# Kernel tuning notes

Hardware: AMD Instinct MI355X
Metric: run time of the kernel (lower is better)

The kernel has to match this reference:

```python
import jax, jax.numpy as jnp
import numpy as np

NUM_HEADS = 4
HEAD_DIM = 64
BN_EPS = 1e-5


def setup_inputs() -> dict:
    key = jax.random.key(0)
    ks = jax.random.split(key, 6)
    B, C, H, W = 8, 256, 48, 48
    HD = NUM_HEADS * HEAD_DIM  # 256
    x = jax.random.normal(ks[0], (B, C, H, W), dtype=jnp.float32)
    q_w = jax.random.normal(ks[1], (HD, C), dtype=jnp.float32) * (1.0 / np.sqrt(C))
    k_w = jax.random.normal(ks[2], (HEAD_DIM, C), dtype=jnp.float32) * (1.0 / np.sqrt(C))
    v_w = jax.random.normal(ks[3], (HEAD_DIM, C), dtype=jnp.float32) * (1.0 / np.sqrt(C))
    proj_w = jax.random.normal(ks[4], (C, HD), dtype=jnp.float32) * (1.0 / np.sqrt(HD))
    proj_b = jnp.zeros((C,), dtype=jnp.float32)
    gamma = jnp.ones((C,), dtype=jnp.float32)
    beta = jnp.zeros((C,), dtype=jnp.float32)
    return {"x": x, "q_w": q_w, "k_w": k_w, "v_w": v_w,
            "proj_w": proj_w, "proj_b": proj_b, "gamma": gamma, "beta": beta}


def reference(x, q_w, k_w, v_w, proj_w, proj_b, gamma, beta):
    B, C, H, W = x.shape
    N = H * W
    scale = HEAD_DIM ** -0.5
    xf = x.reshape(B, C, N)  # 1x1 conv == channel matmul
    q = jnp.einsum('oc,bcn->bon', q_w, xf).reshape(B, NUM_HEADS, HEAD_DIM, N)
    k = jnp.einsum('dc,bcn->bdn', k_w, xf)  # shared single KV head (MQA)
    v = jnp.einsum('dc,bcn->bdn', v_w, xf)
    # scores: [B, heads, N, N]
    attn = jnp.einsum('bhdn,bdm->bhnm', q, k) * scale
    attn = jax.nn.softmax(attn, axis=-1)
    out = jnp.einsum('bhnm,bdm->bhdn', attn, v)  # [B, heads, d, N]
    out = out.reshape(B, NUM_HEADS * HEAD_DIM, N)
    out = jnp.einsum('co,bon->bcn', proj_w, out) + proj_b[None, :, None]
    out = out.reshape(B, C, H, W)
    # BatchNorm2d (training-mode batch statistics, biased variance)
    mean = jnp.mean(out, axis=(0, 2, 3), keepdims=True)
    var = jnp.var(out, axis=(0, 2, 3), keepdims=True)
    out = gamma[None, :, None, None] * (out - mean) * jax.lax.rsqrt(var + BN_EPS) + beta[None, :, None, None]
    return out + x
```

## Files before the change

kernel.cpp:

```cpp
#include <hip/hip_runtime.h>
#include <hip/hip_bf16.h>
#include <math.h>

#define BB 8
#define CCH 256
#define NN 2304
#define NH 4
#define HDIM 64
#define QKV_ROWS 384
#define BN_EPS 1e-5f
#define NTILES 36
#define NPART 288
#define SLOG2E 0.18033688011112042f

typedef short bf16x8 __attribute__((ext_vector_type(8)));
typedef short bf16x4 __attribute__((ext_vector_type(4)));
typedef float f32x4 __attribute__((ext_vector_type(4)));

#if __has_builtin(__builtin_amdgcn_exp2f)
#define EXP2(x) __builtin_amdgcn_exp2f(x)
#else
#define EXP2(x) __expf((x) * 0.6931471805599453f)
#endif

#define MFMA32(a, b, c) __builtin_amdgcn_mfma_f32_16x16x32_bf16(a, b, c, 0, 0, 0)

__device__ __forceinline__ unsigned bfpair(float a, float b) {
    __hip_bfloat162 h = __float22bfloat162_rn(make_float2(a, b));
    return *(unsigned*)&h;
}
__device__ __forceinline__ unsigned short f2bf(float f) {
    unsigned u = __float_as_uint(f);
    u = (u + 0x7FFFu + ((u >> 16) & 1u)) >> 16;
    return (unsigned short)u;
}
__device__ __forceinline__ float bf2f(unsigned short s) {
    return __uint_as_float((unsigned)s << 16);
}

__global__ __launch_bounds__(256) void prep_k(
    const float* __restrict__ x,
    const float* __restrict__ qw, const float* __restrict__ kw,
    const float* __restrict__ vw, const float* __restrict__ pw,
    unsigned short* __restrict__ xT, unsigned short* __restrict__ xb,
    unsigned short* __restrict__ Wb, unsigned short* __restrict__ Pb)
{
    const int bid = blockIdx.x;
    const int tid = threadIdx.x;
    if (bid < 1152) {
        __shared__ float sX[64][65];
        const int b  = bid / 144;
        const int rem = bid - b * 144;
        const int nb = (rem >> 2) * 64;
        const int cb = (rem & 3) * 64;

        #pragma unroll
        for (int u = 0; u < 4; ++u) {
            int c  = (tid >> 4) + 16 * u;
            int n4 = (tid & 15) * 4;
            float4 v = *(const float4*)(x + ((size_t)(b * CCH + cb + c)) * NN + nb + n4);
            sX[c][n4+0] = v.x; sX[c][n4+1] = v.y; sX[c][n4+2] = v.z; sX[c][n4+3] = v.w;
        }
        __syncthreads();

        const int n  = tid >> 2;
        const int cg = (tid & 3) * 16;
        unsigned vals[8];
        #pragma unroll
        for (int p = 0; p < 8; ++p)
            vals[p] = bfpair(sX[cg + 2*p][n], sX[cg + 2*p + 1][n]);
        unsigned short* dst = xT + ((size_t)(b * NN + nb + n)) * CCH + cb + cg;
        *(uint4*)dst = make_uint4(vals[0], vals[1], vals[2], vals[3]);
        *(uint4*)(dst + 8) = make_uint4(vals[4], vals[5], vals[6], vals[7]);

        #pragma unroll
        for (int it = 0; it < 2; ++it) {
            int flat = tid + 256 * it;
            int row = flat >> 3;
            int n8  = (flat & 7) * 8;
            unsigned vv[4];
            #pragma unroll
            for (int p = 0; p < 4; ++p)
                vv[p] = bfpair(sX[row][n8 + 2*p], sX[row][n8 + 2*p + 1]);
            *(uint4*)(xb + ((size_t)(b * CCH + cb + row)) * NN + nb + n8) =
                make_uint4(vv[0], vv[1], vv[2], vv[3]);
        }
    } else {
        int idx = (bid - 1152) * 256 + tid;
        if (idx < 98304) {
            int o = idx >> 8, c = idx & 255;
            float v;
            if (o < 256)      v = qw[(size_t)o * CCH + c] * SLOG2E;
            else if (o < 320) v = kw[(size_t)(o - 256) * CCH + c];
            else              v = vw[(size_t)(o - 320) * CCH + c];
            Wb[idx] = f2bf(v);
        } else {
            int j = idx - 98304;
            if (j < 65536) Pb[j] = f2bf(pw[j]);
        }
    }
}

__global__ __launch_bounds__(128) void qkv_mfma_k(
    const unsigned short* __restrict__ Wb, const unsigned short* __restrict__ xT,
    unsigned short* __restrict__ Qt, unsigned short* __restrict__ Kt,
    unsigned short* __restrict__ Vn)
{
    __shared__ unsigned short sE[2][64 * 72];
    const int tid = threadIdx.x;
    const int wave = tid >> 6;
    const int lane = tid & 63;
    const int quad = lane >> 4;
    const int l15  = lane & 15;
    const int b  = blockIdx.x;
    const int nb = blockIdx.y * 64;
    const int mb = blockIdx.z * 128 + wave * 64;

    const unsigned short* Ab = Wb + (size_t)(mb + l15) * CCH + quad * 8;
    const unsigned short* Bb = xT + ((size_t)(b * NN + nb + l15)) * CCH + quad * 8;

    f32x4 C[4][4] = {};
    bf16x8 aA[2][4], bB[2][4];
    #pragma unroll
    for (int i = 0; i < 4; ++i) aA[0][i] = *(const bf16x8*)(Ab + (size_t)(16*i) * CCH);
    #pragma unroll
    for (int j = 0; j < 4; ++j) bB[0][j] = *(const bf16x8*)(Bb + (size_t)(16*j) * CCH);

    #pragma unroll
    for (int kk = 0; kk < 8; ++kk) {
        const int cur = kk & 1;
        if (kk < 7) {
            const int k1 = (kk + 1) * 32;
            #pragma unroll
            for (int i = 0; i < 4; ++i) aA[cur^1][i] = *(const bf16x8*)(Ab + (size_t)(16*i) * CCH + k1);
            #pragma unroll
            for (int j = 0; j < 4; ++j) bB[cur^1][j] = *(const bf16x8*)(Bb + (size_t)(16*j) * CCH + k1);
        }
        #pragma unroll
        for (int i = 0; i < 4; ++i)
            #pragma unroll
            for (int j = 0; j < 4; ++j)
                C[i][j] = MFMA32(aA[cur][i], bB[cur][j], C[i][j]);
    }

    unsigned short* sEw = &sE[wave][0];
    if (mb < 320) {
        #pragma unroll
        for (int i = 0; i < 4; ++i)
            #pragma unroll
            for (int j = 0; j < 4; ++j) {
                unsigned p01 = bfpair(C[i][j][0], C[i][j][1]);
                unsigned p23 = bfpair(C[i][j][2], C[i][j][3]);
                unsigned short* p = sEw + (16*j + l15) * 72 + 16*i + quad*4;
                *(unsigned*)p = p01;
                *(unsigned*)(p + 2) = p23;
            }
        if (mb < 256) {
            #pragma unroll
            for (int it = 0; it < 8; ++it) {
                int flat = lane + 64 * it;
                int row = flat >> 3;
                int o8  = (flat & 7) * 8;
                uint4 v = *(const uint4*)(sEw + row * 72 + o8);
                *(uint4*)(Qt + ((size_t)(b * NN + nb + row)) * CCH + mb + o8) = v;
            }
        } else {
            #pragma unroll
            for (int it = 0; it < 8; ++it) {
                int flat = lane + 64 * it;
                int row = flat >> 3;
                int o8  = (flat & 7) * 8;
                uint4 v = *(const uint4*)(sEw + row * 72 + o8);
                *(uint4*)(Kt + ((size_t)(b * NN + nb + row)) * 64 + o8) = v;
            }
        }
    } else {
        #pragma unroll
        for (int i = 0; i < 4; ++i)
            #pragma unroll
            for (int j = 0; j < 4; ++j) {
                unsigned p01 = bfpair(C[i][j][0], C[i][j][1]);
                unsigned p23 = bfpair(C[i][j][2], C[i][j][3]);
                unsigned short* p = sEw + (16*i + quad*4) * 72 + 16*j + l15;
                p[0]   = (unsigned short)p01;
                p[72]  = (unsigned short)(p01 >> 16);
                p[144] = (unsigned short)p23;
                p[216] = (unsigned short)(p23 >> 16);
            }
        #pragma unroll
        for (int it = 0; it < 8; ++it) {
            int flat = lane + 64 * it;
            int row = flat >> 3;
            int n8  = (flat & 7) * 8;
            uint4 v = *(const uint4*)(sEw + row * 72 + n8);
            *(uint4*)(Vn + ((size_t)(b * 64 + (mb - 320) + row)) * NN + nb + n8) = v;
        }
    }
}

__global__ __launch_bounds__(256, 4) void attn_k(
    const unsigned short* __restrict__ Qt,
    const unsigned short* __restrict__ Kt,
    const unsigned short* __restrict__ Vn,
    unsigned short* __restrict__ Ao)
{
    __shared__ __align__(16) unsigned short sKV[2 * 2 * 64 * 64];

    const int tid   = threadIdx.x;
    const int wave  = tid >> 6;
    const int lane  = tid & 63;
    const int quad  = lane >> 4;
    const int l15   = lane & 15;
    const int qoff  = wave * 32;
    const int b     = blockIdx.x;
    const int nb    = blockIdx.y * 128;
    const int head  = blockIdx.z;

    const bf16x8 vone8 = {(short)0x3F80, (short)0x3F80, (short)0x3F80, (short)0x3F80,
                          (short)0x3F80, (short)0x3F80, (short)0x3F80, (short)0x3F80};

    bf16x8 bQ[2][2];
    const unsigned short* QtB = Qt + ((size_t)(b * NN + nb + qoff + l15)) * CCH + head * 64 + quad * 8;
    #pragma unroll
    for (int qt = 0; qt < 2; ++qt)
        #pragma unroll
        for (int s = 0; s < 2; ++s)
            bQ[qt][s] = *(const bf16x8*)(QtB + (size_t)(16*qt) * CCH + s * 32);

    const int r0  = tid >> 3;
    const int c8  = (tid & 7) * 8;
    const int kr0 = (r0 & 3) | (((r0 >> 3) & 3) << 2) | (((r0 >> 2) & 1) << 4);
    const int kwc = ((tid & 7) ^ (kr0 & 7)) * 8;
    const int vwc = ((tid & 7) ^ (r0 & 7)) * 8;

    const unsigned short* Kb = Kt + ((size_t)(b * NN + r0)) * 64 + c8;
    const unsigned short* Vb = Vn + ((size_t)(b * 64 + r0)) * NN + c8;

    bf16x8 pf[4];
    pf[0] = *(const bf16x8*)(Kb);
    pf[1] = *(const bf16x8*)(Kb + (size_t)32 * 64);
    pf[2] = *(const bf16x8*)(Vb);
    pf[3] = *(const bf16x8*)(Vb + (size_t)32 * NN);
    *(bf16x8*)(sKV + kr0 * 64 + kwc)          = pf[0];
    *(bf16x8*)(sKV + (kr0 + 32) * 64 + kwc)   = pf[1];
    *(bf16x8*)(sKV + 4096 + r0 * 64 + vwc)    = pf[2];
    *(bf16x8*)(sKV + 4096 + (r0 + 32) * 64 + vwc) = pf[3];
    pf[0] = *(const bf16x8*)(Kb + (size_t)64 * 64);
    pf[1] = *(const bf16x8*)(Kb + (size_t)96 * 64);
    pf[2] = *(const bf16x8*)(Vb + 64);
    pf[3] = *(const bf16x8*)(Vb + (size_t)32 * NN + 64);

    f32x4 O[4][2] = {};
    f32x4 dacc[2] = {};

    for (int step = 0; step < NTILES; ++step) {
        const int cur = step & 1;
        __syncthreads();

        if (step + 1 < NTILES) {
            unsigned short* dstb = sKV + (cur ^ 1) * 8192;
            *(bf16x8*)(dstb + kr0 * 64 + kwc)             = pf[0];
            *(bf16x8*)(dstb + (kr0 + 32) * 64 + kwc)      = pf[1];
            *(bf16x8*)(dstb + 4096 + r0 * 64 + vwc)       = pf[2];
            *(bf16x8*)(dstb + 4096 + (r0 + 32) * 64 + vwc) = pf[3];
        }
        if (step + 2 < NTILES) {
            const int keys0 = (step + 2) * 64;
            pf[0] = *(const bf16x8*)(Kb + (size_t)keys0 * 64);
            pf[1] = *(const bf16x8*)(Kb + (size_t)(keys0 + 32) * 64);
            pf[2] = *(const bf16x8*)(Vb + keys0);
            pf[3] = *(const bf16x8*)(Vb + (size_t)32 * NN + keys0);
        }

        const unsigned short* sKb = sKV + cur * 8192;
        const unsigned short* sVb = sKb + 4096;

        f32x4 C[4][2] = {};
        #pragma unroll
        for (int s = 0; s < 2; ++s)
            #pragma unroll
            for (int kt = 0; kt < 4; ++kt) {
                const int row = 16*kt + l15;
                const int chsw = ((s*4 + quad) ^ (row & 7)) * 8;
                bf16x8 aK = *(const bf16x8*)(sKb + row * 64 + chsw);
                C[kt][0] = MFMA32(aK, bQ[0][s], C[kt][0]);
                C[kt][1] = MFMA32(aK, bQ[1][s], C[kt][1]);
            }

        bf16x8 bP[2][2];
        #pragma unroll
        for (int kt2 = 0; kt2 < 2; ++kt2)
            #pragma unroll
            for (int qt = 0; qt < 2; ++qt) {
                union { unsigned u[4]; bf16x8 v; } xp;
                const f32x4 c0 = C[2*kt2][qt];
                const f32x4 c1 = C[2*kt2+1][qt];
                xp.u[0] = bfpair(EXP2(c0[0]), EXP2(c0[1]));
                xp.u[1] = bfpair(EXP2(c0[2]), EXP2(c0[3]));
                xp.u[2] = bfpair(EXP2(c1[0]), EXP2(c1[1]));
                xp.u[3] = bfpair(EXP2(c1[2]), EXP2(c1[3]));
                bP[kt2][qt] = xp.v;
            }

        #pragma unroll
        for (int kt2 = 0; kt2 < 2; ++kt2) {
            dacc[0] = MFMA32(vone8, bP[kt2][0], dacc[0]);
            dacc[1] = MFMA32(vone8, bP[kt2][1], dacc[1]);
        }

        #pragma unroll
        for (int jd = 0; jd < 4; ++jd)
            #pragma unroll
            for (int kt2 = 0; kt2 < 2; ++kt2) {
                const int row = 16*jd + l15;
                const int chsw = ((4*kt2 + quad) ^ (row & 7)) * 8;
                bf16x8 aV = *(const bf16x8*)(sVb + row * 64 + chsw);
                O[jd][0] = MFMA32(aV, bP[kt2][0], O[jd][0]);
                O[jd][1] = MFMA32(aV, bP[kt2][1], O[jd][1]);
            }
    }
    __syncthreads();

    float rinv[2];
    rinv[0] = 1.0f / dacc[0][0];
    rinv[1] = 1.0f / dacc[1][0];
    unsigned short* sT = (unsigned short*)sKV;
    #pragma unroll
    for (int qt = 0; qt < 2; ++qt)
        #pragma unroll
        for (int jd = 0; jd < 4; ++jd) {
            unsigned lo = bfpair(O[jd][qt][0] * rinv[qt], O[jd][qt][1] * rinv[qt]);
            unsigned hi = bfpair(O[jd][qt][2] * rinv[qt], O[jd][qt][3] * rinv[qt]);
            *(uint2*)(sT + (qoff + 16*qt + l15) * 72 + 16*jd + quad*4) = make_uint2(lo, hi);
        }
    __syncthreads();

    #pragma unroll
    for (int it = 0; it < 4; ++it) {
        int flat = tid + 256 * it;
        int row  = flat >> 3;
        int cc8  = (flat & 7) * 8;
        uint4 v = *(const uint4*)(sT + row * 72 + cc8);
        *(uint4*)(Ao + ((size_t)(b * NN + nb + row)) * CCH + head * 64 + cc8) = v;
    }
}

__global__ __launch_bounds__(128) void proj_mfma_k(
    const unsigned short* __restrict__ Pb, const unsigned short* __restrict__ Ao,
    const float* __restrict__ pb, unsigned short* __restrict__ projb,
    float* __restrict__ psum, float* __restrict__ psq)
{
    __shared__ unsigned short sE[2][64 * 72];
    const int tid = threadIdx.x;
    const int wave = tid >> 6;
    const int lane = tid & 63;
    const int quad = lane >> 4;
    const int l15  = lane & 15;
    const int b  = blockIdx.x;
    const int nb = blockIdx.y * 64;
    const int mb = blockIdx.z * 128 + wave * 64;
    const int part = b * NTILES + blockIdx.y;

    const unsigned short* Ab = Pb + (size_t)(mb + l15) * CCH + quad * 8;
    const unsigned short* Bb = Ao + ((size_t)(b * NN + nb + l15)) * CCH + quad * 8;

    f32x4 C[4][4] = {};
    bf16x8 aA[2][4], bB[2][4];
    #pragma unroll
    for (int i = 0; i < 4; ++i) aA[0][i] = *(const bf16x8*)(Ab + (size_t)(16*i) * CCH);
    #pragma unroll
    for (int j = 0; j < 4; ++j) bB[0][j] = *(const bf16x8*)(Bb + (size_t)(16*j) * CCH);

    #pragma unroll
    for (int kk = 0; kk < 8; ++kk) {
        const int cur = kk & 1;
        if (kk < 7) {
            const int k1 = (kk + 1) * 32;
            #pragma unroll
            for (int i = 0; i < 4; ++i) aA[cur^1][i] = *(const bf16x8*)(Ab + (size_t)(16*i) * CCH + k1);
            #pragma unroll
            for (int j = 0; j < 4; ++j) bB[cur^1][j] = *(const bf16x8*)(Bb + (size_t)(16*j) * CCH + k1);
        }
        #pragma unroll
        for (int i = 0; i < 4; ++i)
            #pragma unroll
            for (int j = 0; j < 4; ++j)
                C[i][j] = MFMA32(aA[cur][i], bB[cur][j], C[i][j]);
    }

    unsigned short* sEw = &sE[wave][0];
    #pragma unroll
    for (int i = 0; i < 4; ++i) {
        #pragma unroll
        for (int r = 0; r < 4; ++r) {
            const int ch = mb + 16*i + quad*4 + r;
            const float bias = pb[ch];
            float v0 = C[i][0][r] + bias, v1 = C[i][1][r] + bias;
            float v2 = C[i][2][r] + bias, v3 = C[i][3][r] + bias;
            C[i][0][r] = v0; C[i][1][r] = v1; C[i][2][r] = v2; C[i][3][r] = v3;
            float rs = (v0 + v1) + (v2 + v3);
            float rq = (v0*v0 + v1*v1) + (v2*v2 + v3*v3);
            rs += __shfl_xor(rs, 1); rq += __shfl_xor(rq, 1);
            rs += __shfl_xor(rs, 2); rq += __shfl_xor(rq, 2);
            rs += __shfl_xor(rs, 4); rq += __shfl_xor(rq, 4);
            rs += __shfl_xor(rs, 8); rq += __shfl_xor(rq, 8);
            if (l15 == 0) {
                psum[(size_t)ch * NPART + part] = rs;
                psq [(size_t)ch * NPART + part] = rq;
            }
        }
    }

    #pragma unroll
    for (int i = 0; i < 4; ++i)
        #pragma unroll
        for (int j = 0; j < 4; ++j) {
            unsigned p01 = bfpair(C[i][j][0], C[i][j][1]);
            unsigned p23 = bfpair(C[i][j][2], C[i][j][3]);
            unsigned short* p = sEw + (16*i + quad*4) * 72 + 16*j + l15;
            p[0]   = (unsigned short)p01;
            p[72]  = (unsigned short)(p01 >> 16);
            p[144] = (unsigned short)p23;
            p[216] = (unsigned short)(p23 >> 16);
        }
    #pragma unroll
    for (int it = 0; it < 8; ++it) {
        int flat = lane + 64 * it;
        int row = flat >> 3;
        int n8  = (flat & 7) * 8;
        uint4 v = *(const uint4*)(sEw + row * 72 + n8);
        *(uint4*)(projb + ((size_t)(b * CCH + mb + row)) * NN + nb + n8) = v;
    }
}

__global__ __launch_bounds__(256) void bn_apply_k(
    const unsigned short* __restrict__ projb, const unsigned short* __restrict__ xb,
    const float* __restrict__ psum, const float* __restrict__ psq,
    const float* __restrict__ gamma, const float* __restrict__ beta,
    float* __restrict__ out)
{
    const int tid = threadIdx.x;
    const int b = blockIdx.x;
    const int c = blockIdx.y;

    float s = 0.f, q = 0.f;
    for (int k = tid; k < NPART; k += 256) {
        s += psum[(size_t)c * NPART + k];
        q += psq [(size_t)c * NPART + k];
    }
    __shared__ float rs[256], rq[256];
    rs[tid] = s; rq[tid] = q;
    __syncthreads();
    for (int off = 128; off > 0; off >>= 1) {
        if (tid < off) { rs[tid] += rs[tid + off]; rq[tid] += rq[tid + off]; }
        __syncthreads();
    }
    const float inv_n = 1.0f / (float)(BB * NN);
    float mean = rs[0] * inv_n;
    float var  = rq[0] * inv_n - mean * mean;
    float scv = gamma[c] * rsqrtf(var + BN_EPS);
    float shv = beta[c] - mean * scv;

    #pragma unroll
    for (int it = 0; it < 2; ++it) {
        int chunk = tid + 256 * it;
        if (chunk < 288) {
            size_t base = ((size_t)(b * CCH + c)) * NN + chunk * 8;
            uint4 pv = *(const uint4*)(projb + base);
            uint4 xv = *(const uint4*)(xb + base);
            const unsigned short* pp = (const unsigned short*)&pv;
            const unsigned short* xx = (const unsigned short*)&xv;
            float4 r0, r1;
            r0.x = scv * bf2f(pp[0]) + shv + bf2f(xx[0]);
            r0.y = scv * bf2f(pp[1]) + shv + bf2f(xx[1]);
            r0.z = scv * bf2f(pp[2]) + shv + bf2f(xx[2]);
            r0.w = scv * bf2f(pp[3]) + shv + bf2f(xx[3]);
            r1.x = scv * bf2f(pp[4]) + shv + bf2f(xx[4]);
            r1.y = scv * bf2f(pp[5]) + shv + bf2f(xx[5]);
            r1.z = scv * bf2f(pp[6]) + shv + bf2f(xx[6]);
            r1.w = scv * bf2f(pp[7]) + shv + bf2f(xx[7]);
            *(float4*)(out + base) = r0;
            *(float4*)(out + base + 4) = r1;
        }
    }
}

extern "C" void kernel_launch(void* const* d_in, const int* in_sizes, int n_in,
                              void* d_out, int out_size, void* d_ws, size_t ws_size,
                              hipStream_t stream)
{
    const float* x     = (const float*)d_in[0];
    const float* qw    = (const float*)d_in[1];
    const float* kw    = (const float*)d_in[2];
    const float* vw    = (const float*)d_in[3];
    const float* pw    = (const float*)d_in[4];
    const float* pb    = (const float*)d_in[5];
    const float* gamma = (const float*)d_in[6];
    const float* beta  = (const float*)d_in[7];
    float* out = (float*)d_out;

    char* ws = (char*)d_ws;
    unsigned short* xT = (unsigned short*)ws;
    unsigned short* Ao = (unsigned short*)ws;
    unsigned short* Wb = (unsigned short*)(ws + 9437184);
    unsigned short* Pb = (unsigned short*)(ws + 9633792);
    unsigned short* Qt = (unsigned short*)(ws + 9764864);
    unsigned short* Kt = (unsigned short*)(ws + 19202048);
    unsigned short* Vn = (unsigned short*)(ws + 21561344);
    unsigned short* projb = (unsigned short*)(ws + 9764864);
    float* psum  = (float*)(ws + 28639232);
    float* psq   = (float*)(ws + 28934144);
    unsigned short* xb = (unsigned short*)(ws + 29229056);

    prep_k<<<1792, 256, 0, stream>>>(x, qw, kw, vw, pw, xT, xb, Wb, Pb);

    dim3 g1(BB, NN / 64, 3);
    qkv_mfma_k<<<g1, 128, 0, stream>>>(Wb, xT, Qt, Kt, Vn);

    dim3 g2(BB, NN / 128, NH);
    attn_k<<<g2, 256, 0, stream>>>(Qt, Kt, Vn, Ao);

    dim3 g3(BB, NN / 64, 2);
    proj_mfma_k<<<g3, 128, 0, stream>>>(Pb, Ao, pb, projb, psum, psq);

    dim3 g4(BB, CCH);
    bn_apply_k<<<g4, 256, 0, stream>>>(projb, xb, psum, psq, gamma, beta, out);
}
```

Baseline: 193.6 us.

## Software-pipeline attention loop: overlap previous PV MFMAs with current QK and exp

```diff
diff --git a/kernel.cpp b/kernel.cpp
--- a/kernel.cpp
+++ b/kernel.cpp
@@ -198,13 +198,76 @@
     }
 }
 
-__global__ __launch_bounds__(256, 4) void attn_k(
+#define ATT_STEP(STEPN, KCUR, KNXT, VPRV, VNXT, BPP, BPN, DOPV)                  \
+    {                                                                            \
+        __syncthreads();                                                         \
+        if ((STEPN) + 1 < NTILES) {                                              \
+            *(bf16x8*)(sKV + (KNXT) + kr0 * 64 + kwc)        = pf[0];            \
+            *(bf16x8*)(sKV + (KNXT) + (kr0 + 32) * 64 + kwc) = pf[1];            \
+            *(bf16x8*)(sKV + (VNXT) + r0 * 64 + vwc)         = pf[2];            \
+            *(bf16x8*)(sKV + (VNXT) + (r0 + 32) * 64 + vwc)  = pf[3];            \
+        }                                                                        \
+        if ((STEPN) + 2 < NTILES) {                                              \
+            const int keys0_ = ((STEPN) + 2) * 64;                               \
+            pf[0] = *(const bf16x8*)(Kb + (size_t)keys0_ * 64);                  \
+            pf[1] = *(const bf16x8*)(Kb + (size_t)(keys0_ + 32) * 64);           \
+            pf[2] = *(const bf16x8*)(Vb + keys0_);                               \
+            pf[3] = *(const bf16x8*)(Vb + (size_t)32 * NN + keys0_);             \
+        }                                                                        \
+        if (DOPV) {                                                              \
+            _Pragma("unroll")                                                    \
+            for (int jd_ = 0; jd_ < 4; ++jd_) {                                  \
+                _Pragma("unroll")                                                \
+                for (int kt2_ = 0; kt2_ < 2; ++kt2_) {                           \
+                    const int row_ = 16 * jd_ + l15;                             \
+                    const int ch_ = ((4 * kt2_ + quad) ^ (row_ & 7)) * 8;        \
+                    bf16x8 aV_ = *(const bf16x8*)(sKV + (VPRV) + row_ * 64 + ch_);\
+                    O[jd_][0] = MFMA32(aV_, BPP[kt2_][0], O[jd_][0]);            \
+                    O[jd_][1] = MFMA32(aV_, BPP[kt2_][1], O[jd_][1]);            \
+                }                                                                \
+            }                                                                    \
+            dacc[0] = MFMA32(vone8, BPP[0][0], dacc[0]);                         \
+            dacc[1] = MFMA32(vone8, BPP[0][1], dacc[1]);                         \
+            dacc[0] = MFMA32(vone8, BPP[1][0], dacc[0]);                         \
+            dacc[1] = MFMA32(vone8, BPP[1][1], dacc[1]);                         \
+        }                                                                        \
+        f32x4 C_[4][2] = {};                                                     \
+        _Pragma("unroll")                                                        \
+        for (int s_ = 0; s_ < 2; ++s_) {                                         \
+            _Pragma("unroll")                                                    \
+            for (int kt_ = 0; kt_ < 4; ++kt_) {                                  \
+                const int row_ = 16 * kt_ + l15;                                 \
+                const int ch_ = ((s_ * 4 + quad) ^ (row_ & 7)) * 8;              \
+                bf16x8 aK_ = *(const bf16x8*)(sKV + (KCUR) + row_ * 64 + ch_);   \
+                C_[kt_][0] = MFMA32(aK_, bQ[0][s_], C_[kt_][0]);                 \
+                C_[kt_][1] = MFMA32(aK_, bQ[1][s_], C_[kt_][1]);                 \
+            }                                                                    \
+        }                                                                        \
+        _Pragma("unroll")                                                        \
+        for (int kt2_ = 0; kt2_ < 2; ++kt2_) {                                   \
+            _Pragma("unroll")                                                    \
+            for (int qt_ = 0; qt_ < 2; ++qt_) {                                  \
+                union { unsigned u[4]; bf16x8 v; } xp_;                          \
+                const f32x4 c0_ = C_[2 * kt2_][qt_];                             \
+                const f32x4 c1_ = C_[2 * kt2_ + 1][qt_];                         \
+                xp_.u[0] = bfpair(EXP2(c0_[0]), EXP2(c0_[1]));                   \
+                xp_.u[1] = bfpair(EXP2(c0_[2]), EXP2(c0_[3]));                   \
+                xp_.u[2] = bfpair(EXP2(c1_[0]), EXP2(c1_[1]));                   \
+                xp_.u[3] = bfpair(EXP2(c1_[2]), EXP2(c1_[3]));                   \
+                BPN[kt2_][qt_] = xp_.v;                                          \
+            }                                                                    \
+        }                                                                        \
+    }
+
+#define ROTV(x) x = ((x) == 16384) ? 8192 : (x) + 4096
+
+__global__ __launch_bounds__(256, 3) void attn_k(
     const unsigned short* __restrict__ Qt,
     const unsigned short* __restrict__ Kt,
     const unsigned short* __restrict__ Vn,
     unsigned short* __restrict__ Ao)
 {
-    __shared__ __align__(16) unsigned short sKV[2 * 2 * 64 * 64];
+    __shared__ __align__(16) unsigned short sKV[20480];
 
     const int tid   = threadIdx.x;
     const int wave  = tid >> 6;
@@ -241,10 +304,10 @@
     pf[1] = *(const bf16x8*)(Kb + (size_t)32 * 64);
     pf[2] = *(const bf16x8*)(Vb);
     pf[3] = *(const bf16x8*)(Vb + (size_t)32 * NN);
-    *(bf16x8*)(sKV + kr0 * 64 + kwc)          = pf[0];
-    *(bf16x8*)(sKV + (kr0 + 32) * 64 + kwc)   = pf[1];
-    *(bf16x8*)(sKV + 4096 + r0 * 64 + vwc)    = pf[2];
-    *(bf16x8*)(sKV + 4096 + (r0 + 32) * 64 + vwc) = pf[3];
+    *(bf16x8*)(sKV + kr0 * 64 + kwc)               = pf[0];
+    *(bf16x8*)(sKV + (kr0 + 32) * 64 + kwc)        = pf[1];
+    *(bf16x8*)(sKV + 8192 + r0 * 64 + vwc)         = pf[2];
+    *(bf16x8*)(sKV + 8192 + (r0 + 32) * 64 + vwc)  = pf[3];
     pf[0] = *(const bf16x8*)(Kb + (size_t)64 * 64);
     pf[1] = *(const bf16x8*)(Kb + (size_t)96 * 64);
     pf[2] = *(const bf16x8*)(Vb + 64);
@@ -252,73 +315,36 @@
 
     f32x4 O[4][2] = {};
     f32x4 dacc[2] = {};
-
-    for (int step = 0; step < NTILES; ++step) {
-        const int cur = step & 1;
-        __syncthreads();
-
-        if (step + 1 < NTILES) {
-            unsigned short* dstb = sKV + (cur ^ 1) * 8192;
-            *(bf16x8*)(dstb + kr0 * 64 + kwc)             = pf[0];
-            *(bf16x8*)(dstb + (kr0 + 32) * 64 + kwc)      = pf[1];
-            *(bf16x8*)(dstb + 4096 + r0 * 64 + vwc)       = pf[2];
-            *(bf16x8*)(dstb + 4096 + (r0 + 32) * 64 + vwc) = pf[3];
-        }
-        if (step + 2 < NTILES) {
-            const int keys0 = (step + 2) * 64;
-            pf[0] = *(const bf16x8*)(Kb + (size_t)keys0 * 64);
-            pf[1] = *(const bf16x8*)(Kb + (size_t)(keys0 + 32) * 64);
-            pf[2] = *(const bf16x8*)(Vb + keys0);
-            pf[3] = *(const bf16x8*)(Vb + (size_t)32 * NN + keys0);
-        }
-
-        const unsigned short* sKb = sKV + cur * 8192;
-        const unsigned short* sVb = sKb + 4096;
-
-        f32x4 C[4][2] = {};
-        #pragma unroll
-        for (int s = 0; s < 2; ++s)
-            #pragma unroll
-            for (int kt = 0; kt < 4; ++kt) {
-                const int row = 16*kt + l15;
-                const int chsw = ((s*4 + quad) ^ (row & 7)) * 8;
-                bf16x8 aK = *(const bf16x8*)(sKb + row * 64 + chsw);
-                C[kt][0] = MFMA32(aK, bQ[0][s], C[kt][0]);
-                C[kt][1] = MFMA32(aK, bQ[1][s], C[kt][1]);
-            }
-
-        bf16x8 bP[2][2];
-        #pragma unroll
-        for (int kt2 = 0; kt2 < 2; ++kt2)
-            #pragma unroll
-            for (int qt = 0; qt < 2; ++qt) {
-                union { unsigned u[4]; bf16x8 v; } xp;
-                const f32x4 c0 = C[2*kt2][qt];
-                const f32x4 c1 = C[2*kt2+1][qt];
-                xp.u[0] = bfpair(EXP2(c0[0]), EXP2(c0[1]));
-                xp.u[1] = bfpair(EXP2(c0[2]), EXP2(c0[3]));
-                xp.u[2] = bfpair(EXP2(c1[0]), EXP2(c1[1]));
-                xp.u[3] = bfpair(EXP2(c1[2]), EXP2(c1[3]));
-                bP[kt2][qt] = xp.v;
-            }
-
+    bf16x8 bPe[2][2], bPo[2][2];
+
+    ATT_STEP(0, 0, 4096, 0 , 12288, bPo , bPe, 0);
+
+    int vPrv = 8192;
+    int vNxt = 16384;
+    for (int sp = 1; sp < 35; sp += 2) {
+        ATT_STEP(sp,     4096, 0,    vPrv, vNxt, bPe, bPo, 1);
+        ROTV(vPrv); ROTV(vNxt);
+        ATT_STEP(sp + 1, 0,    4096, vPrv, vNxt, bPo, bPe, 1);
+        ROTV(vPrv); ROTV(vNxt);
+    }
+    ATT_STEP(35, 4096, 0, vPrv, vNxt, bPe, bPo, 1);
+    ROTV(vPrv);
+
+    #pragma unroll
+    for (int jd = 0; jd < 4; ++jd)
         #pragma unroll
         for (int kt2 = 0; kt2 < 2; ++kt2) {
-            dacc[0] = MFMA32(vone8, bP[kt2][0], dacc[0]);
-            dacc[1] = MFMA32(vone8, bP[kt2][1], dacc[1]);
-        }
-
-        #pragma unroll
-        for (int jd = 0; jd < 4; ++jd)
-            #pragma unroll
-            for (int kt2 = 0; kt2 < 2; ++kt2) {
-                const int row = 16*jd + l15;
-                const int chsw = ((4*kt2 + quad) ^ (row & 7)) * 8;
-                bf16x8 aV = *(const bf16x8*)(sVb + row * 64 + chsw);
-                O[jd][0] = MFMA32(aV, bP[kt2][0], O[jd][0]);
-                O[jd][1] = MFMA32(aV, bP[kt2][1], O[jd][1]);
-            }
-    }
+            const int row = 16*jd + l15;
+            const int ch  = ((4*kt2 + quad) ^ (row & 7)) * 8;
+            bf16x8 aV = *(const bf16x8*)(sKV + vPrv + row * 64 + ch);
+            O[jd][0] = MFMA32(aV, bPo[kt2][0], O[jd][0]);
+            O[jd][1] = MFMA32(aV, bPo[kt2][1], O[jd][1]);
+        }
+    dacc[0] = MFMA32(vone8, bPo[0][0], dacc[0]);
+    dacc[1] = MFMA32(vone8, bPo[0][1], dacc[1]);
+    dacc[0] = MFMA32(vone8, bPo[1][0], dacc[0]);
+    dacc[1] = MFMA32(vone8, bPo[1][1], dacc[1]);
+
     __syncthreads();
 
     float rinv[2];
```

New measurement: 190.2 us. No clear change (-1.8%).

## Load K/V tiles directly from global memory into registers, dropping LDS staging

Applied to the files above, without the earlier changes.

```diff
diff --git a/kernel.cpp b/kernel.cpp
--- a/kernel.cpp
+++ b/kernel.cpp
@@ -198,13 +198,13 @@
     }
 }
 
-__global__ __launch_bounds__(256, 4) void attn_k(
+__global__ __launch_bounds__(256, 3) void attn_k(
     const unsigned short* __restrict__ Qt,
     const unsigned short* __restrict__ Kt,
     const unsigned short* __restrict__ Vn,
     unsigned short* __restrict__ Ao)
 {
-    __shared__ __align__(16) unsigned short sKV[2 * 2 * 64 * 64];
+    __shared__ __align__(16) unsigned short sT[128 * 72];
 
     const int tid   = threadIdx.x;
     const int wave  = tid >> 6;
@@ -227,64 +227,32 @@
         for (int s = 0; s < 2; ++s)
             bQ[qt][s] = *(const bf16x8*)(QtB + (size_t)(16*qt) * CCH + s * 32);
 
-    const int r0  = tid >> 3;
-    const int c8  = (tid & 7) * 8;
-    const int kr0 = (r0 & 3) | (((r0 >> 3) & 3) << 2) | (((r0 >> 2) & 1) << 4);
-    const int kwc = ((tid & 7) ^ (kr0 & 7)) * 8;
-    const int vwc = ((tid & 7) ^ (r0 & 7)) * 8;
-
-    const unsigned short* Kb = Kt + ((size_t)(b * NN + r0)) * 64 + c8;
-    const unsigned short* Vb = Vn + ((size_t)(b * 64 + r0)) * NN + c8;
-
-    bf16x8 pf[4];
-    pf[0] = *(const bf16x8*)(Kb);
-    pf[1] = *(const bf16x8*)(Kb + (size_t)32 * 64);
-    pf[2] = *(const bf16x8*)(Vb);
-    pf[3] = *(const bf16x8*)(Vb + (size_t)32 * NN);
-    *(bf16x8*)(sKV + kr0 * 64 + kwc)          = pf[0];
-    *(bf16x8*)(sKV + (kr0 + 32) * 64 + kwc)   = pf[1];
-    *(bf16x8*)(sKV + 4096 + r0 * 64 + vwc)    = pf[2];
-    *(bf16x8*)(sKV + 4096 + (r0 + 32) * 64 + vwc) = pf[3];
-    pf[0] = *(const bf16x8*)(Kb + (size_t)64 * 64);
-    pf[1] = *(const bf16x8*)(Kb + (size_t)96 * 64);
-    pf[2] = *(const bf16x8*)(Vb + 64);
-    pf[3] = *(const bf16x8*)(Vb + (size_t)32 * NN + 64);
+    const int kbasel = (l15 & 3) | (((l15 >> 2) & 3) << 3);
+    const unsigned short* Kp = Kt + (size_t)b * NN * 64;
+    const unsigned short* Vp = Vn + (size_t)b * 64 * NN;
 
     f32x4 O[4][2] = {};
     f32x4 dacc[2] = {};
 
+    #pragma unroll 4
     for (int step = 0; step < NTILES; ++step) {
-        const int cur = step & 1;
-        __syncthreads();
-
-        if (step + 1 < NTILES) {
-            unsigned short* dstb = sKV + (cur ^ 1) * 8192;
-            *(bf16x8*)(dstb + kr0 * 64 + kwc)             = pf[0];
-            *(bf16x8*)(dstb + (kr0 + 32) * 64 + kwc)      = pf[1];
-            *(bf16x8*)(dstb + 4096 + r0 * 64 + vwc)       = pf[2];
-            *(bf16x8*)(dstb + 4096 + (r0 + 32) * 64 + vwc) = pf[3];
-        }
-        if (step + 2 < NTILES) {
-            const int keys0 = (step + 2) * 64;
-            pf[0] = *(const bf16x8*)(Kb + (size_t)keys0 * 64);
-            pf[1] = *(const bf16x8*)(Kb + (size_t)(keys0 + 32) * 64);
-            pf[2] = *(const bf16x8*)(Vb + keys0);
-            pf[3] = *(const bf16x8*)(Vb + (size_t)32 * NN + keys0);
-        }
-
-        const unsigned short* sKb = sKV + cur * 8192;
-        const unsigned short* sVb = sKb + 4096;
-
+        const int k0 = step * 64;
+
+        bf16x8 aK[2][4];
+        #pragma unroll
+        for (int s = 0; s < 2; ++s)
+            #pragma unroll
+            for (int kt = 0; kt < 4; ++kt) {
+                const int krow = kbasel + ((kt & 1) << 2) + ((kt >> 1) << 5);
+                aK[s][kt] = *(const bf16x8*)(Kp + (size_t)(k0 + krow) * 64 + s * 32 + quad * 8);
+            }
         f32x4 C[4][2] = {};
         #pragma unroll
         for (int s = 0; s < 2; ++s)
             #pragma unroll
             for (int kt = 0; kt < 4; ++kt) {
-                const int row = 16*kt + l15;
-                const int chsw = ((s*4 + quad) ^ (row & 7)) * 8;
-                bf16x8 aK = *(const bf16x8*)(sKb + row * 64 + chsw);
-                C[kt][0] = MFMA32(aK, bQ[0][s], C[kt][0]);
-                C[kt][1] = MFMA32(aK, bQ[1][s], C[kt][1]);
+                C[kt][0] = MFMA32(aK[s][kt], bQ[0][s], C[kt][0]);
+                C[kt][1] = MFMA32(aK[s][kt], bQ[1][s], C[kt][1]);
             }
 
         bf16x8 bP[2][2];
@@ -302,6 +270,13 @@
                 bP[kt2][qt] = xp.v;
             }
 
+        bf16x8 aV[4][2];
+        #pragma unroll
+        for (int jd = 0; jd < 4; ++jd)
+            #pragma unroll
+            for (int kt2 = 0; kt2 < 2; ++kt2)
+                aV[jd][kt2] = *(const bf16x8*)(Vp + (size_t)(16*jd + l15) * NN + k0 + (4*kt2 + quad) * 8);
+
         #pragma unroll
         for (int kt2 = 0; kt2 < 2; ++kt2) {
             dacc[0] = MFMA32(vone8, bP[kt2][0], dacc[0]);
@@ -312,19 +287,14 @@
         for (int jd = 0; jd < 4; ++jd)
             #pragma unroll
             for (int kt2 = 0; kt2 < 2; ++kt2) {
-                const int row = 16*jd + l15;
-                const int chsw = ((4*kt2 + quad) ^ (row & 7)) * 8;
-                bf16x8 aV = *(const bf16x8*)(sVb + row * 64 + chsw);
-                O[jd][0] = MFMA32(aV, bP[kt2][0], O[jd][0]);
-                O[jd][1] = MFMA32(aV, bP[kt2][1], O[jd][1]);
-            }
-    }
-    __syncthreads();
+                O[jd][0] = MFMA32(aV[jd][kt2], bP[kt2][0], O[jd][0]);
+                O[jd][1] = MFMA32(aV[jd][kt2], bP[kt2][1], O[jd][1]);
+            }
+    }
 
     float rinv[2];
     rinv[0] = 1.0f / dacc[0][0];
     rinv[1] = 1.0f / dacc[1][0];
-    unsigned short* sT = (unsigned short*)sKV;
     #pragma unroll
     for (int qt = 0; qt < 2; ++qt)
         #pragma unroll
```

After: 323.3 us. +67.0%, slower.
